# Kernel tuning notes

Hardware: AMD Instinct MI355X
Metric: run time of the kernel (lower is better)

Reference implementation:

```python
import jax, jax.numpy as jnp
import numpy as np

VOCAB, EMBED, HIDDEN, NCLS = 32000, 512, 1024, 1000
BATCH, SEQ = 128, 512


def setup_inputs() -> dict:
    key = jax.random.key(0)
    ks = jax.random.split(key, 8)
    s_in = 1.0 / np.sqrt(EMBED + HIDDEN)
    s_h = 1.0 / np.sqrt(HIDDEN)
    return {
        "x": jax.random.randint(ks[0], (BATCH, SEQ), 0, VOCAB, dtype=jnp.int32),
        "emb": jax.random.normal(ks[1], (VOCAB, EMBED), dtype=jnp.float32),
        "Wz": jax.random.uniform(ks[2], (EMBED + HIDDEN, HIDDEN), jnp.float32, -s_in, s_in),
        "bz": jax.random.uniform(ks[3], (HIDDEN,), jnp.float32, -s_in, s_in),
        "Wh": jax.random.uniform(ks[4], (EMBED + HIDDEN, HIDDEN), jnp.float32, -s_in, s_in),
        "bh": jax.random.uniform(ks[5], (HIDDEN,), jnp.float32, -s_in, s_in),
        "Wfc": jax.random.uniform(ks[6], (HIDDEN, NCLS), jnp.float32, -s_h, s_h),
        "bfc": jax.random.uniform(ks[7], (NCLS,), jnp.float32, -s_h, s_h),
    }


def reference(x, emb, Wz, bz, Wh, bh, Wfc, bfc):
    # embedding lookup: [B, S, E]
    e = emb[x]
    B = x.shape[0]
    h0 = jnp.zeros((B, Wz.shape[1]), dtype=emb.dtype)

    def step(h, x_t):
        c = jnp.concatenate([x_t, h], axis=1)          # [B, E+H]
        z = jax.nn.sigmoid(c @ Wz + bz)                # forget/update gate
        h_tilde = jnp.tanh(c @ Wh + bh)                # candidate state
        h_new = (1.0 - z) * h + z * h_tilde
        return h_new, None

    h_final, _ = jax.lax.scan(step, h0, jnp.swapaxes(e, 0, 1))  # scan over S
    return h_final @ Wfc + bfc                          # logits [B, NCLS]
```

## Files before the change

kernel.cpp:

```cpp
#include <hip/hip_runtime.h>

#define BATCH 128
#define SEQ   512
#define EMB   512
#define HID   1024
#define KC    1536
#define NCLS  1000
#define NBLK  128
#define TPB   512

using short8 = __attribute__((ext_vector_type(8))) short;
using f32x4  = __attribute__((ext_vector_type(4))) float;
typedef unsigned long long u64;

__device__ __forceinline__ short f2bf(float f) {
    unsigned u = __float_as_uint(f);
    unsigned r = (u + 0x7fffu + ((u >> 16) & 1u)) >> 16;
    return (short)r;
}
__device__ __forceinline__ float bf2f(short s) {
    unsigned u = ((unsigned)(unsigned short)s) << 16;
    return __uint_as_float(u);
}

#define OFF_CH0 0u
#define OFF_CL0 262144u
#define OFF_BAR 524288u
#define OFF_CH1 526336u
#define OFF_CL1 788480u
#define OFF_H   1050624u
#define ZERO_I4 32896u

__global__ void mgu_init(int4* __restrict__ ws4) {
    unsigned i = blockIdx.x * blockDim.x + threadIdx.x;
    if (i < ZERO_I4) ws4[i] = make_int4(0, 0, 0, 0);
}

__global__ __launch_bounds__(TPB, 1) void mgu_scan(
    const int* __restrict__ x, const float* __restrict__ emb,
    const float* __restrict__ Wz, const float* __restrict__ bz,
    const float* __restrict__ Wh, const float* __restrict__ bh,
    short* __restrict__ ch0, short* __restrict__ cl0,
    short* __restrict__ ch1, short* __restrict__ cl1,
    unsigned* __restrict__ bars, float* __restrict__ h)
{
    __shared__ short As[16][1544];
    __shared__ short Al[16][1032];

    const int tid  = threadIdx.x;
    const int w    = tid >> 6;
    const int lane = tid & 63;
    const int q    = lane >> 4;
    const int n    = lane & 15;
    const int blk  = blockIdx.x;
    const int r0   = (blk >> 4) << 4;
    const int j0   = (((blk & 15) << 3) + w) << 3;
    unsigned* bar  = bars + ((blk >> 4) << 6);

    const float* Wg = (n < 8) ? Wz : Wh;
    const float* wp = Wg + j0 + (n & 7);
    short8 Bf[48];
#pragma unroll
    for (int ks = 0; ks < 48; ++ks) {
        short8 f;
#pragma unroll
        for (int i = 0; i < 8; ++i)
            f[i] = f2bf(wp[(long)(ks * 32 + q * 8 + i) * HID]);
        Bf[ks] = f;
    }
    const float bzv = bz[j0 + (n & 7)];
    const float bhv = bh[j0 + (n & 7)];

    float hreg[4] = {0.f, 0.f, 0.f, 0.f};

    const int hrow = tid >> 5;
    const int hc0  = (tid & 31) << 4;

    auto stage_emb = [&](int tt) {
        int tok = x[(r0 + hrow) * SEQ + tt];
        const float4* ep = (const float4*)(emb + (long)tok * EMB + hc0);
        float4 e0 = ep[0], e1 = ep[1], e2 = ep[2], e3 = ep[3];
        short8 s0, s1;
        s0[0] = f2bf(e0.x); s0[1] = f2bf(e0.y); s0[2] = f2bf(e0.z); s0[3] = f2bf(e0.w);
        s0[4] = f2bf(e1.x); s0[5] = f2bf(e1.y); s0[6] = f2bf(e1.z); s0[7] = f2bf(e1.w);
        s1[0] = f2bf(e2.x); s1[1] = f2bf(e2.y); s1[2] = f2bf(e2.z); s1[3] = f2bf(e2.w);
        s1[4] = f2bf(e3.x); s1[5] = f2bf(e3.y); s1[6] = f2bf(e3.z); s1[7] = f2bf(e3.w);
        *(short8*)&As[hrow][hc0]     = s0;
        *(short8*)&As[hrow][hc0 + 8] = s1;
    };

    stage_emb(0);

    for (int t = 0; t < SEQ; ++t) {
        const short* chR = (t & 1) ? ch1 : ch0;
        const short* clR = (t & 1) ? cl1 : cl0;
        short*       chW = (t & 1) ? ch0 : ch1;
        short*       clW = (t & 1) ? cl0 : cl1;

        u64 hv[8], lv[8];
#pragma unroll
        for (int k2 = 0; k2 < 8; ++k2) {
            int idx = tid + (k2 << 9);
            int row = idx >> 8;
            int wc  = idx & 255;
            const u64* hp8 = (const u64*)(chR + (r0 + row) * HID);
            const u64* lp8 = (const u64*)(clR + (r0 + row) * HID);
            hv[k2] = __hip_atomic_load(hp8 + wc, __ATOMIC_RELAXED, __HIP_MEMORY_SCOPE_AGENT);
            lv[k2] = __hip_atomic_load(lp8 + wc, __ATOMIC_RELAXED, __HIP_MEMORY_SCOPE_AGENT);
        }
#pragma unroll
        for (int k2 = 0; k2 < 8; ++k2) {
            int idx = tid + (k2 << 9);
            int row = idx >> 8;
            int wc  = idx & 255;
            *(u64*)&As[row][512 + (wc << 2)] = hv[k2];
            *(u64*)&Al[row][wc << 2]         = lv[k2];
        }
        __syncthreads();

        const short* ap  = &As[n][q * 8];
        const short* alp = &Al[n][q * 8];
        f32x4 a0 = {0.f,0.f,0.f,0.f}, a1 = a0, a2 = a0, a3 = a0;
#pragma unroll
        for (int ks = 0; ks < 48; ks += 4) {
            short8 f0 = *(const short8*)(ap + (ks + 0) * 32);
            short8 f1 = *(const short8*)(ap + (ks + 1) * 32);
            short8 f2 = *(const short8*)(ap + (ks + 2) * 32);
            short8 f3 = *(const short8*)(ap + (ks + 3) * 32);
            a0 = __builtin_amdgcn_mfma_f32_16x16x32_bf16(f0, Bf[ks + 0], a0, 0, 0, 0);
            a1 = __builtin_amdgcn_mfma_f32_16x16x32_bf16(f1, Bf[ks + 1], a1, 0, 0, 0);
            a2 = __builtin_amdgcn_mfma_f32_16x16x32_bf16(f2, Bf[ks + 2], a2, 0, 0, 0);
            a3 = __builtin_amdgcn_mfma_f32_16x16x32_bf16(f3, Bf[ks + 3], a3, 0, 0, 0);
        }
#pragma unroll
        for (int e = 0; e < 32; e += 4) {
            short8 g0 = *(const short8*)(alp + (e + 0) * 32);
            short8 g1 = *(const short8*)(alp + (e + 1) * 32);
            short8 g2 = *(const short8*)(alp + (e + 2) * 32);
            short8 g3 = *(const short8*)(alp + (e + 3) * 32);
            a0 = __builtin_amdgcn_mfma_f32_16x16x32_bf16(g0, Bf[16 + e + 0], a0, 0, 0, 0);
            a1 = __builtin_amdgcn_mfma_f32_16x16x32_bf16(g1, Bf[16 + e + 1], a1, 0, 0, 0);
            a2 = __builtin_amdgcn_mfma_f32_16x16x32_bf16(g2, Bf[16 + e + 2], a2, 0, 0, 0);
            a3 = __builtin_amdgcn_mfma_f32_16x16x32_bf16(g3, Bf[16 + e + 3], a3, 0, 0, 0);
        }
        f32x4 acc = (a0 + a1) + (a2 + a3);

        float o0 = __shfl_xor(acc[0], 8, 64);
        float o1 = __shfl_xor(acc[1], 8, 64);
        float o2 = __shfl_xor(acc[2], 8, 64);
        float o3 = __shfl_xor(acc[3], 8, 64);

        if (n < 8) {
            float zp[4] = {acc[0], acc[1], acc[2], acc[3]};
            float tp[4] = {o0, o1, o2, o3};
            const int j = j0 + n;
#pragma unroll
            for (int r2 = 0; r2 < 4; ++r2) {
                float z  = 1.f / (1.f + __expf(-(zp[r2] + bzv)));
                float ht = tanhf(tp[r2] + bhv);
                float ho = hreg[r2];
                float hn = ho + z * (ht - ho);
                hreg[r2] = hn;
                int rr = (r0 + q * 4 + r2) * HID + j;
                if (t < SEQ - 1) {
                    short hi = f2bf(hn);
                    __hip_atomic_store(chW + rr, hi, __ATOMIC_RELAXED, __HIP_MEMORY_SCOPE_AGENT);
                    __hip_atomic_store(clW + rr, f2bf(hn - bf2f(hi)), __ATOMIC_RELAXED, __HIP_MEMORY_SCOPE_AGENT);
                } else {
                    h[rr] = hn;
                }
            }
        }

        if (t < SEQ - 1) {
            __syncthreads();
            if (tid == 0)
                __hip_atomic_fetch_add(bar, 1u, __ATOMIC_RELAXED, __HIP_MEMORY_SCOPE_AGENT);
            stage_emb(t + 1);
            if (tid == 0) {
                unsigned tgt = (unsigned)(t + 1) * 16u;
                while (__hip_atomic_load(bar, __ATOMIC_RELAXED, __HIP_MEMORY_SCOPE_AGENT) < tgt)
                    __builtin_amdgcn_s_sleep(1);
            }
            __syncthreads();
        }
    }
}

__global__ __launch_bounds__(256) void mgu_fc(const float* __restrict__ h,
                                              const float* __restrict__ Wfc,
                                              const float* __restrict__ bfc,
                                              float* __restrict__ out) {
    __shared__ float hs[BATCH][65];
    const int tid = threadIdx.x;
    const int n0  = blockIdx.x * 8;
    const int b   = tid & 127;
    const int nn  = tid >> 7;
    const int nc  = n0 + nn * 4;
    float acc0 = 0.f, acc1 = 0.f, acc2 = 0.f, acc3 = 0.f;

    for (int k0 = 0; k0 < HID; k0 += 64) {
        __syncthreads();
#pragma unroll
        for (int jj = 0; jj < 8; ++jj) {
            int idx = tid + jj * 256;
            int bb  = idx >> 4;
            int kk  = (idx & 15) << 2;
            const float4 v = *(const float4*)(h + bb * HID + k0 + kk);
            hs[bb][kk] = v.x; hs[bb][kk + 1] = v.y; hs[bb][kk + 2] = v.z; hs[bb][kk + 3] = v.w;
        }
        __syncthreads();
#pragma unroll 8
        for (int k = 0; k < 64; ++k) {
            float hv = hs[b][k];
            const float4 wv = *(const float4*)(Wfc + (long)(k0 + k) * NCLS + nc);
            acc0 += hv * wv.x; acc1 += hv * wv.y; acc2 += hv * wv.z; acc3 += hv * wv.w;
        }
    }
    float* op = out + b * NCLS + nc;
    op[0] = acc0 + bfc[nc + 0];
    op[1] = acc1 + bfc[nc + 1];
    op[2] = acc2 + bfc[nc + 2];
    op[3] = acc3 + bfc[nc + 3];
}

extern "C" void kernel_launch(void* const* d_in, const int* in_sizes, int n_in,
                              void* d_out, int out_size, void* d_ws, size_t ws_size,
                              hipStream_t stream) {
    const int*   x   = (const int*)  d_in[0];
    const float* emb = (const float*)d_in[1];
    const float* Wz  = (const float*)d_in[2];
    const float* bz  = (const float*)d_in[3];
    const float* Wh  = (const float*)d_in[4];
    const float* bh  = (const float*)d_in[5];
    const float* Wfc = (const float*)d_in[6];
    const float* bfc = (const float*)d_in[7];
    float* out = (float*)d_out;

    char* ws = (char*)d_ws;
    short*    ch0  = (short*)   (ws + OFF_CH0);
    short*    cl0  = (short*)   (ws + OFF_CL0);
    unsigned* bars = (unsigned*)(ws + OFF_BAR);
    short*    ch1  = (short*)   (ws + OFF_CH1);
    short*    cl1  = (short*)   (ws + OFF_CL1);
    float*    h    = (float*)   (ws + OFF_H);

    mgu_init<<<129, 256, 0, stream>>>((int4*)ws);

    mgu_scan<<<NBLK, TPB, 0, stream>>>(x, emb, Wz, bz, Wh, bh,
                                       ch0, cl0, ch1, cl1, bars, h);

    mgu_fc<<<125, 256, 0, stream>>>(h, Wfc, bfc, out);
}
```

Before: 3.524 ms.

## Split K across waves with per-wave A fragments loaded directly to registers

Each wave now owns a slice of the reduction dimension for all 64 output columns of the block, instead of the full K for 8 columns. A fragments (embedding and h hi/lo) are loaded straight from global into registers, which removes the LDS staging of A and the barrier before the MFMAs. Partial sums are then reduced across the 8 waves through an LDS buffer. The intent is to cut LDS traffic and per-step latency on the sequential critical path, at the cost of an extra cross-wave LDS reduction and 8 accumulators per wave.

```diff
diff --git a/kernel.cpp b/kernel.cpp
--- a/kernel.cpp
+++ b/kernel.cpp
@@ -4,7 +4,6 @@
 #define SEQ   512
 #define EMB   512
 #define HID   1024
-#define KC    1536
 #define NCLS  1000
 #define NBLK  128
 #define TPB   512
@@ -21,6 +20,17 @@
 __device__ __forceinline__ float bf2f(short s) {
     unsigned u = ((unsigned)(unsigned short)s) << 16;
     return __uint_as_float(u);
+}
+__device__ __forceinline__ short8 pack8(float4 a, float4 b) {
+    short8 s;
+    s[0] = f2bf(a.x); s[1] = f2bf(a.y); s[2] = f2bf(a.z); s[3] = f2bf(a.w);
+    s[4] = f2bf(b.x); s[5] = f2bf(b.y); s[6] = f2bf(b.z); s[7] = f2bf(b.w);
+    return s;
+}
+__device__ __forceinline__ short8 mk8(u64 lo, u64 hi) {
+    union { u64 d[2]; short8 s; } u;
+    u.d[0] = lo; u.d[1] = hi;
+    return u.s;
 }
 
 #define OFF_CH0 0u
@@ -44,8 +54,7 @@
     short* __restrict__ ch1, short* __restrict__ cl1,
     unsigned* __restrict__ bars, float* __restrict__ h)
 {
-    __shared__ short As[16][1544];
-    __shared__ short Al[16][1032];
+    __shared__ f32x4 Rbuf[8][8][64];
 
     const int tid  = threadIdx.x;
     const int w    = tid >> 6;
@@ -54,42 +63,44 @@
     const int n    = lane & 15;
     const int blk  = blockIdx.x;
     const int r0   = (blk >> 4) << 4;
-    const int j0   = (((blk & 15) << 3) + w) << 3;
+    const int jb   = (blk & 15) << 6;
+    const int j0   = jb + (w << 3);
     unsigned* bar  = bars + ((blk >> 4) << 6);
 
     const float* Wg = (n < 8) ? Wz : Wh;
-    const float* wp = Wg + j0 + (n & 7);
     short8 Bf[48];
 #pragma unroll
-    for (int ks = 0; ks < 48; ++ks) {
-        short8 f;
-#pragma unroll
-        for (int i = 0; i < 8; ++i)
-            f[i] = f2bf(wp[(long)(ks * 32 + q * 8 + i) * HID]);
-        Bf[ks] = f;
+    for (int c = 0; c < 8; ++c) {
+#pragma unroll
+        for (int m = 0; m < 6; ++m) {
+            const float* wp = Wg + jb + (c << 3) + (n & 7);
+            short8 f;
+#pragma unroll
+            for (int i = 0; i < 8; ++i)
+                f[i] = f2bf(wp[(long)((w + 8 * m) * 32 + q * 8 + i) * HID]);
+            Bf[c * 6 + m] = f;
+        }
     }
     const float bzv = bz[j0 + (n & 7)];
     const float bhv = bh[j0 + (n & 7)];
 
     float hreg[4] = {0.f, 0.f, 0.f, 0.f};
 
-    const int hrow = tid >> 5;
-    const int hc0  = (tid & 31) << 4;
-
-    auto stage_emb = [&](int tt) {
-        int tok = x[(r0 + hrow) * SEQ + tt];
-        const float4* ep = (const float4*)(emb + (long)tok * EMB + hc0);
-        float4 e0 = ep[0], e1 = ep[1], e2 = ep[2], e3 = ep[3];
-        short8 s0, s1;
-        s0[0] = f2bf(e0.x); s0[1] = f2bf(e0.y); s0[2] = f2bf(e0.z); s0[3] = f2bf(e0.w);
-        s0[4] = f2bf(e1.x); s0[5] = f2bf(e1.y); s0[6] = f2bf(e1.z); s0[7] = f2bf(e1.w);
-        s1[0] = f2bf(e2.x); s1[1] = f2bf(e2.y); s1[2] = f2bf(e2.z); s1[3] = f2bf(e2.w);
-        s1[4] = f2bf(e3.x); s1[5] = f2bf(e3.y); s1[6] = f2bf(e3.z); s1[7] = f2bf(e3.w);
-        *(short8*)&As[hrow][hc0]     = s0;
-        *(short8*)&As[hrow][hc0 + 8] = s1;
-    };
-
-    stage_emb(0);
+    const int xrow = (r0 + n) * SEQ;
+    const int hoff = (r0 + n) * HID + (w << 5) + (q << 3);
+    const int eoff = (w << 5) + (q << 3);
+
+    short8 fe0, fe1;
+    {
+        int tok = x[xrow];
+        const float* ep = emb + (long)tok * EMB + eoff;
+        float4 a0 = *(const float4*)(ep);
+        float4 a1 = *(const float4*)(ep + 4);
+        float4 b0 = *(const float4*)(ep + 256);
+        float4 b1 = *(const float4*)(ep + 260);
+        fe0 = pack8(a0, a1);
+        fe1 = pack8(b0, b1);
+    }
 
     for (int t = 0; t < SEQ; ++t) {
         const short* chR = (t & 1) ? ch1 : ch0;
@@ -97,67 +108,67 @@
         short*       chW = (t & 1) ? ch0 : ch1;
         short*       clW = (t & 1) ? cl0 : cl1;
 
-        u64 hv[8], lv[8];
-#pragma unroll
-        for (int k2 = 0; k2 < 8; ++k2) {
-            int idx = tid + (k2 << 9);
-            int row = idx >> 8;
-            int wc  = idx & 255;
-            const u64* hp8 = (const u64*)(chR + (r0 + row) * HID);
-            const u64* lp8 = (const u64*)(clR + (r0 + row) * HID);
-            hv[k2] = __hip_atomic_load(hp8 + wc, __ATOMIC_RELAXED, __HIP_MEMORY_SCOPE_AGENT);
-            lv[k2] = __hip_atomic_load(lp8 + wc, __ATOMIC_RELAXED, __HIP_MEMORY_SCOPE_AGENT);
-        }
-#pragma unroll
-        for (int k2 = 0; k2 < 8; ++k2) {
-            int idx = tid + (k2 << 9);
-            int row = idx >> 8;
-            int wc  = idx & 255;
-            *(u64*)&As[row][512 + (wc << 2)] = hv[k2];
-            *(u64*)&Al[row][wc << 2]         = lv[k2];
-        }
+        int tok_nxt = x[xrow + ((t < SEQ - 1) ? t + 1 : t)];
+
+        u64 hh[8], ll[8];
+#pragma unroll
+        for (int mm = 0; mm < 4; ++mm) {
+            const u64* hp = (const u64*)(chR + hoff + (mm << 8));
+            hh[2 * mm]     = __hip_atomic_load(hp,     __ATOMIC_RELAXED, __HIP_MEMORY_SCOPE_AGENT);
+            hh[2 * mm + 1] = __hip_atomic_load(hp + 1, __ATOMIC_RELAXED, __HIP_MEMORY_SCOPE_AGENT);
+        }
+#pragma unroll
+        for (int mm = 0; mm < 4; ++mm) {
+            const u64* lp = (const u64*)(clR + hoff + (mm << 8));
+            ll[2 * mm]     = __hip_atomic_load(lp,     __ATOMIC_RELAXED, __HIP_MEMORY_SCOPE_AGENT);
+            ll[2 * mm + 1] = __hip_atomic_load(lp + 1, __ATOMIC_RELAXED, __HIP_MEMORY_SCOPE_AGENT);
+        }
+
+        f32x4 acc[8];
+#pragma unroll
+        for (int c = 0; c < 8; ++c) acc[c] = (f32x4){0.f, 0.f, 0.f, 0.f};
+
+#pragma unroll
+        for (int c = 0; c < 8; ++c)
+            acc[c] = __builtin_amdgcn_mfma_f32_16x16x32_bf16(fe0, Bf[c * 6 + 0], acc[c], 0, 0, 0);
+#pragma unroll
+        for (int c = 0; c < 8; ++c)
+            acc[c] = __builtin_amdgcn_mfma_f32_16x16x32_bf16(fe1, Bf[c * 6 + 1], acc[c], 0, 0, 0);
+
+#pragma unroll
+        for (int mm = 0; mm < 4; ++mm) {
+            short8 fh = mk8(hh[2 * mm], hh[2 * mm + 1]);
+#pragma unroll
+            for (int c = 0; c < 8; ++c)
+                acc[c] = __builtin_amdgcn_mfma_f32_16x16x32_bf16(fh, Bf[c * 6 + 2 + mm], acc[c], 0, 0, 0);
+        }
+#pragma unroll
+        for (int mm = 0; mm < 4; ++mm) {
+            short8 fl = mk8(ll[2 * mm], ll[2 * mm + 1]);
+#pragma unroll
+            for (int c = 0; c < 8; ++c)
+                acc[c] = __builtin_amdgcn_mfma_f32_16x16x32_bf16(fl, Bf[c * 6 + 2 + mm], acc[c], 0, 0, 0);
+        }
+
+#pragma unroll
+        for (int c = 0; c < 8; ++c) Rbuf[w][c][lane] = acc[c];
         __syncthreads();
-
-        const short* ap  = &As[n][q * 8];
-        const short* alp = &Al[n][q * 8];
-        f32x4 a0 = {0.f,0.f,0.f,0.f}, a1 = a0, a2 = a0, a3 = a0;
-#pragma unroll
-        for (int ks = 0; ks < 48; ks += 4) {
-            short8 f0 = *(const short8*)(ap + (ks + 0) * 32);
-            short8 f1 = *(const short8*)(ap + (ks + 1) * 32);
-            short8 f2 = *(const short8*)(ap + (ks + 2) * 32);
-            short8 f3 = *(const short8*)(ap + (ks + 3) * 32);
-            a0 = __builtin_amdgcn_mfma_f32_16x16x32_bf16(f0, Bf[ks + 0], a0, 0, 0, 0);
-            a1 = __builtin_amdgcn_mfma_f32_16x16x32_bf16(f1, Bf[ks + 1], a1, 0, 0, 0);
-            a2 = __builtin_amdgcn_mfma_f32_16x16x32_bf16(f2, Bf[ks + 2], a2, 0, 0, 0);
-            a3 = __builtin_amdgcn_mfma_f32_16x16x32_bf16(f3, Bf[ks + 3], a3, 0, 0, 0);
-        }
-#pragma unroll
-        for (int e = 0; e < 32; e += 4) {
-            short8 g0 = *(const short8*)(alp + (e + 0) * 32);
-            short8 g1 = *(const short8*)(alp + (e + 1) * 32);
-            short8 g2 = *(const short8*)(alp + (e + 2) * 32);
-            short8 g3 = *(const short8*)(alp + (e + 3) * 32);
-            a0 = __builtin_amdgcn_mfma_f32_16x16x32_bf16(g0, Bf[16 + e + 0], a0, 0, 0, 0);
-            a1 = __builtin_amdgcn_mfma_f32_16x16x32_bf16(g1, Bf[16 + e + 1], a1, 0, 0, 0);
-            a2 = __builtin_amdgcn_mfma_f32_16x16x32_bf16(g2, Bf[16 + e + 2], a2, 0, 0, 0);
-            a3 = __builtin_amdgcn_mfma_f32_16x16x32_bf16(g3, Bf[16 + e + 3], a3, 0, 0, 0);
-        }
-        f32x4 acc = (a0 + a1) + (a2 + a3);
-
-        float o0 = __shfl_xor(acc[0], 8, 64);
-        float o1 = __shfl_xor(acc[1], 8, 64);
-        float o2 = __shfl_xor(acc[2], 8, 64);
-        float o3 = __shfl_xor(acc[3], 8, 64);
+        f32x4 r = Rbuf[0][w][lane];
+#pragma unroll
+        for (int w2 = 1; w2 < 8; ++w2) r += Rbuf[w2][w][lane];
+
+        float oarr[4];
+        oarr[0] = __shfl_xor(r[0], 8, 64);
+        oarr[1] = __shfl_xor(r[1], 8, 64);
+        oarr[2] = __shfl_xor(r[2], 8, 64);
+        oarr[3] = __shfl_xor(r[3], 8, 64);
 
         if (n < 8) {
-            float zp[4] = {acc[0], acc[1], acc[2], acc[3]};
-            float tp[4] = {o0, o1, o2, o3};
             const int j = j0 + n;
 #pragma unroll
             for (int r2 = 0; r2 < 4; ++r2) {
-                float z  = 1.f / (1.f + __expf(-(zp[r2] + bzv)));
-                float ht = tanhf(tp[r2] + bhv);
+                float z  = 1.f / (1.f + __expf(-(r[r2] + bzv)));
+                float ht = tanhf(oarr[r2] + bhv);
                 float ho = hreg[r2];
                 float hn = ho + z * (ht - ho);
                 hreg[r2] = hn;
@@ -176,7 +187,15 @@
             __syncthreads();
             if (tid == 0)
                 __hip_atomic_fetch_add(bar, 1u, __ATOMIC_RELAXED, __HIP_MEMORY_SCOPE_AGENT);
-            stage_emb(t + 1);
+            {
+                const float* ep = emb + (long)tok_nxt * EMB + eoff;
+                float4 a0 = *(const float4*)(ep);
+                float4 a1 = *(const float4*)(ep + 4);
+                float4 b0 = *(const float4*)(ep + 256);
+                float4 b1 = *(const float4*)(ep + 260);
+                fe0 = pack8(a0, a1);
+                fe1 = pack8(b0, b1);
+            }
             if (tid == 0) {
                 unsigned tgt = (unsigned)(t + 1) * 16u;
                 while (__hip_atomic_load(bar, __ATOMIC_RELAXED, __HIP_MEMORY_SCOPE_AGENT) < tgt)
```

After: 4.276 ms. +21.3%, slower.
